# Kernel optimization log

Measured on AMD Instinct MI355X. Metric: run time of the kernel, lower is better.

The kernel has to match this reference:

```python
import math
import jax, jax.numpy as jnp
import numpy as np

N_HEADS = 16
D_EMBED = 1024
D_HEAD = D_EMBED // N_HEADS
B, S = 4, 2048


def setup_inputs() -> dict:
    key = jax.random.key(0)
    k1, k2, k3, k4, k5 = jax.random.split(key, 5)
    scale_in = 1.0 / math.sqrt(D_EMBED)
    return {
        "x": jax.random.normal(k1, (B, S, D_EMBED), dtype=jnp.float32),
        "w_in": jax.random.normal(k2, (3 * D_EMBED, D_EMBED), dtype=jnp.float32) * scale_in,
        "b_in": jax.random.normal(k3, (3 * D_EMBED,), dtype=jnp.float32) * 0.02,
        "w_out": jax.random.normal(k4, (D_EMBED, D_EMBED), dtype=jnp.float32) * scale_in,
        "b_out": jax.random.normal(k5, (D_EMBED,), dtype=jnp.float32) * 0.02,
        "causal_mask": 1,
    }


def reference(x, w_in, b_in, w_out, b_out, causal_mask):
    Bn, Sn, D = x.shape
    # fused QKV projection (torch Linear: x @ W.T + b)
    qkv = x @ w_in.T + b_in                       # (B, S, 3D)
    q, k, v = jnp.split(qkv, 3, axis=-1)
    def to_heads(t):
        return t.reshape(Bn, Sn, N_HEADS, D_HEAD).transpose(0, 2, 1, 3)  # (B,H,S,dh)
    q, k, v = to_heads(q), to_heads(k), to_heads(v)
    # manual scaled dot-product attention, full (B,H,S,S) scores
    scores = jnp.einsum("bhqd,bhkd->bhqk", q, k)
    if causal_mask:
        tri = jnp.triu(jnp.ones((Sn, Sn), dtype=bool), k=1)
        scores = jnp.where(tri, -jnp.inf, scores)
    scores = scores / math.sqrt(D_HEAD)
    weights = jax.nn.softmax(scores, axis=-1)
    out = jnp.einsum("bhqk,bhkd->bhqd", weights, v)  # (B,H,S,dh)
    out = out.transpose(0, 2, 1, 3).reshape(Bn, Sn, D)
    return out @ w_out.T + b_out
```

## Files before the change

### kernel.cpp

```cpp
#include <hip/hip_runtime.h>

typedef __bf16 bf16x8 __attribute__((ext_vector_type(8)));
typedef float  f32x4  __attribute__((ext_vector_type(4)));
typedef unsigned int uint;

__device__ inline unsigned short f2bf(float f) {
  union { float f; unsigned int u; } v; v.f = f;
  unsigned int u = v.u;
  unsigned int r = u + 0x7FFF + ((u >> 16) & 1);
  return (unsigned short)(r >> 16);
}

__device__ inline uint pack_bf16_rhu(float a, float b) {
  uint ua = __builtin_bit_cast(uint, a) + 0x8000u;
  uint ub = __builtin_bit_cast(uint, b) + 0x8000u;
  return __builtin_amdgcn_perm(ub, ua, 0x07060302u);
}

__device__ inline void load_lds16(const unsigned short* g, unsigned short* l) {
  __builtin_amdgcn_global_load_lds(
      (const __attribute__((address_space(1))) uint*)(g),
      (__attribute__((address_space(3))) uint*)(l), 16, 0, 0);
}

__device__ inline void cvt4(const float* in, unsigned short* out) {
  float4 f = *reinterpret_cast<const float4*>(in);
  ushort4 o;
  o.x = f2bf(f.x); o.y = f2bf(f.y); o.z = f2bf(f.z); o.w = f2bf(f.w);
  *reinterpret_cast<ushort4*>(out) = o;
}

__global__ void cvt_all(const float* __restrict__ x, const float* __restrict__ w_in,
                        const float* __restrict__ w_out,
                        unsigned short* __restrict__ x_bf,
                        unsigned short* __restrict__ w_in_bf,
                        unsigned short* __restrict__ w_out_bf) {
  const int n1 = 8192 * 1024, n2 = 3072 * 1024;
  int i = (blockIdx.x * blockDim.x + threadIdx.x) * 4;
  if (i < n1)            cvt4(x + i, x_bf + i);
  else if (i < n1 + n2)  cvt4(w_in + (i - n1), w_in_bf + (i - n1));
  else                   cvt4(w_out + (i - n1 - n2), w_out_bf + (i - n1 - n2));
}

template<bool OUT_BF16, bool VSPLIT>
__global__ __launch_bounds__(256) void gemm_bt128(
    const unsigned short* __restrict__ A,
    const unsigned short* __restrict__ B,
    const float* __restrict__ bias,
    void* __restrict__ Cout,
    unsigned short* __restrict__ vt,
    int M, int N, int K, int ldc, float scale, int ncut)
{
  __shared__ __attribute__((aligned(16))) unsigned short As[128 * 64];
  __shared__ __attribute__((aligned(16))) unsigned short Bs[128 * 64];

  const int t    = threadIdx.x;
  const int wave = t >> 6, lane = t & 63;
  const int l16  = lane & 15, quad = lane >> 4;
  const int wr = wave >> 1, wc = wave & 1;
  const int m0 = blockIdx.y * 128, n0 = blockIdx.x * 128;
  const int l8 = l16 & 7;

  f32x4 acc[4][4] = {};

  for (int k0 = 0; k0 < K; k0 += 64) {
#pragma unroll
    for (int i = 0; i < 4; ++i) {
      int chunk = i * 256 + t;
      int row = chunk >> 3, cb = chunk & 7;
      int gcb = cb ^ (row & 7);
      load_lds16(A + (size_t)(m0 + row) * K + k0 + gcb * 8, As + chunk * 8);
    }
#pragma unroll
    for (int i = 0; i < 4; ++i) {
      int chunk = i * 256 + t;
      int row = chunk >> 3, cb = chunk & 7;
      int gcb = cb ^ (row & 7);
      load_lds16(B + (size_t)(n0 + row) * K + k0 + gcb * 8, Bs + chunk * 8);
    }
    __syncthreads();
#pragma unroll
    for (int ks = 0; ks < 2; ++ks) {
      bf16x8 af[4], bfr[4];
#pragma unroll
      for (int mt = 0; mt < 4; ++mt)
        af[mt] = *(const bf16x8*)(As + (wr * 64 + mt * 16 + l16) * 64 +
                                  (((ks * 4 + quad) ^ l8) << 3));
#pragma unroll
      for (int nt = 0; nt < 4; ++nt)
        bfr[nt] = *(const bf16x8*)(Bs + (wc * 64 + nt * 16 + l16) * 64 +
                                   (((ks * 4 + quad) ^ l8) << 3));
#pragma unroll
      for (int mt = 0; mt < 4; ++mt)
#pragma unroll
        for (int nt = 0; nt < 4; ++nt)
          acc[mt][nt] = __builtin_amdgcn_mfma_f32_16x16x32_bf16(af[mt], bfr[nt], acc[mt][nt], 0, 0, 0);
    }
    __syncthreads();
  }

#pragma unroll
  for (int nt = 0; nt < 4; ++nt) {
    int col = n0 + wc * 64 + nt * 16 + l16;
    float bv = bias[col];
    float mlt = (col < ncut) ? scale : 1.0f;
#pragma unroll
    for (int mt = 0; mt < 4; ++mt) {
      int row0 = m0 + wr * 64 + mt * 16 + quad * 4;
      float v0 = (acc[mt][nt][0] + bv) * mlt;
      float v1 = (acc[mt][nt][1] + bv) * mlt;
      float v2 = (acc[mt][nt][2] + bv) * mlt;
      float v3 = (acc[mt][nt][3] + bv) * mlt;
      if (VSPLIT && col >= 2048) {
        int d = col - 2048, h = d >> 6, dd = d & 63;
        int bb = row0 >> 11, s = row0 & 2047;
        uint2 w;
        w.x = pack_bf16_rhu(v0, v1);
        w.y = pack_bf16_rhu(v2, v3);
        *(uint2*)(vt + ((size_t)((bb * 16 + h) * 64 + dd) * 2048 + s)) = w;
      } else {
#pragma unroll
        for (int r = 0; r < 4; ++r) {
          float v = (r == 0) ? v0 : (r == 1) ? v1 : (r == 2) ? v2 : v3;
          if (OUT_BF16)
            ((unsigned short*)Cout)[(size_t)(row0 + r) * ldc + col] = f2bf(v);
          else
            ((float*)Cout)[(size_t)(row0 + r) * ldc + col] = v;
        }
      }
    }
  }
}

__global__ __launch_bounds__(512) void attn(
    const unsigned short* __restrict__ qkv2,
    const unsigned short* __restrict__ vt,
    unsigned short* __restrict__ y,
    const int* __restrict__ flag)
{
  __shared__ __attribute__((aligned(16))) unsigned short Qs[128 * 64];
  __shared__ __attribute__((aligned(16))) unsigned short Ks[2][64 * 64];
  __shared__ __attribute__((aligned(16))) unsigned short Vs[2][64 * 64];

  const int t    = threadIdx.x;
  const int wave = t >> 6, lane = t & 63;
  const int l16  = lane & 15, quad = lane >> 4;
  const int l8   = l16 & 7;
  const int idx  = blockIdx.x;
  const int bh   = idx & 63;
  const int pair = idx >> 6;
  const int b = bh >> 4, h = bh & 15;
  const int causal = flag[0];

  const unsigned short* Qg  = qkv2 + (size_t)b * 2048 * 2048 + h * 64;
  const unsigned short* Kg  = Qg + 1024;
  const unsigned short* Vtg = vt + (size_t)bh * 64 * 2048;

  const int sr = t >> 2, sg = (t & 3) * 2;
  const int slot0 = sr * 64 + (((sg    ) ^ (sr & 7)) << 3);
  const int slot1 = sr * 64 + (((sg + 1) ^ (sr & 7)) << 3);
  const int kr = t >> 3, kg = t & 7;
  const int kslot = kr * 64 + ((kg ^ (kr & 7)) << 3);

  unsigned short* Ps = Qs;

  for (int half = 0; half < 2; ++half) {
    const int qt = half ? pair : (15 - pair);
    const int q0 = qt * 128;
    const int jmax = causal ? 2 * qt + 1 : 31;

    const unsigned short* kptr = Kg + (size_t)kr * 2048 + kg * 8;
    const unsigned short* vptr = Vtg + (size_t)kr * 2048 + kg * 8;
    uint4 kreg = *(const uint4*)kptr;
    uint4 vreg = *(const uint4*)vptr;
    {
      const unsigned short* src = Qg + (size_t)(q0 + sr) * 2048 + sg * 8;
      *(uint4*)(Qs + slot0) = *(const uint4*)src;
      *(uint4*)(Qs + slot1) = *(const uint4*)(src + 8);
    }
    __syncthreads();
    bf16x8 qf[2];
    qf[0] = *(const bf16x8*)(Qs + (wave * 16 + l16) * 64 + (((0 + quad) ^ l8) << 3));
    qf[1] = *(const bf16x8*)(Qs + (wave * 16 + l16) * 64 + (((4 + quad) ^ l8) << 3));
    __syncthreads();

    *(uint4*)(Ks[0] + kslot) = kreg;
    *(uint4*)(Vs[0] + kslot) = vreg;
    kptr += 64 * 2048;
    vptr += 64;
    if (jmax > 0) {
      kreg = *(const uint4*)kptr;
      vreg = *(const uint4*)vptr;
    }
    __syncthreads();

    f32x4 ot[4] = {};
    float l_lane = 0.f;
    const int q_glob = q0 + wave * 16 + l16;
    const int wq_max = q0 + wave * 16 + 15;

    for (int j = 0; j <= jmax; ++j) {
      const int cur = j & 1;
      if (j < jmax) {
        *(uint4*)(Ks[cur ^ 1] + kslot) = kreg;
        *(uint4*)(Vs[cur ^ 1] + kslot) = vreg;
        if (j + 1 < jmax) {
          kptr += 64 * 2048;
          vptr += 64;
          kreg = *(const uint4*)kptr;
          vreg = *(const uint4*)vptr;
        }
      }

      const bool active = !causal || ((j << 6) <= wq_max);
      if (active) {
        f32x4 st[4] = {};
        __builtin_amdgcn_s_setprio(1);
#pragma unroll
        for (int ks = 0; ks < 2; ++ks) {
#pragma unroll
          for (int mt = 0; mt < 4; ++mt) {
            bf16x8 kf = *(const bf16x8*)(Ks[cur] + (mt * 16 + l16) * 64 +
                                         (((ks * 4 + quad) ^ l8) << 3));
            st[mt] = __builtin_amdgcn_mfma_f32_16x16x32_bf16(kf, qf[ks], st[mt], 0, 0, 0);
          }
        }
        __builtin_amdgcn_s_setprio(0);

        const int kv0 = j << 6;
        const bool diag = (causal != 0) && (kv0 + 63 > q_glob);
#pragma unroll
        for (int mt = 0; mt < 4; ++mt) {
          float p[4];
#pragma unroll
          for (int r = 0; r < 4; ++r) {
            float pv = __builtin_amdgcn_exp2f(st[mt][r]);
            if (diag) {
              int kv = kv0 + mt * 16 + quad * 4 + r;
              if (kv > q_glob) pv = 0.f;
            }
            p[r] = pv;
          }
          l_lane += (p[0] + p[1]) + (p[2] + p[3]);
          uint2 w;
          w.x = pack_bf16_rhu(p[0], p[1]);
          w.y = pack_bf16_rhu(p[2], p[3]);
          *(uint2*)(Ps + (wave * 16 + l16) * 64 +
                    ((((mt * 2 + (quad >> 1)) ^ l8) << 3) + (quad & 1) * 4)) = w;
        }
        __threadfence_block();

        __builtin_amdgcn_s_setprio(1);
#pragma unroll
        for (int ks = 0; ks < 2; ++ks) {
          bf16x8 pf = *(const bf16x8*)(Ps + (wave * 16 + l16) * 64 +
                                       (((ks * 4 + quad) ^ l8) << 3));
#pragma unroll
          for (int mt = 0; mt < 4; ++mt) {
            bf16x8 vf = *(const bf16x8*)(Vs[cur] + (mt * 16 + l16) * 64 +
                                         (((ks * 4 + quad) ^ l8) << 3));
            ot[mt] = __builtin_amdgcn_mfma_f32_16x16x32_bf16(vf, pf, ot[mt], 0, 0, 0);
          }
        }
        __builtin_amdgcn_s_setprio(0);
      }
      __syncthreads();
    }

    l_lane += __shfl_xor(l_lane, 16);
    l_lane += __shfl_xor(l_lane, 32);
    float inv = 1.f / l_lane;

#pragma unroll
    for (int mt = 0; mt < 4; ++mt) {
      uint2 w;
      w.x = pack_bf16_rhu(ot[mt][0] * inv, ot[mt][1] * inv);
      w.y = pack_bf16_rhu(ot[mt][2] * inv, ot[mt][3] * inv);
      *(uint2*)(Ps + (wave * 16 + l16) * 64 +
                ((((mt * 2 + (quad >> 1)) ^ l8) << 3) + (quad & 1) * 4)) = w;
    }
    __syncthreads();
    {
      size_t base = ((size_t)b * 2048 + q0 + sr) * 1024 + h * 64 + sg * 8;
      *(uint4*)(y + base)     = *(const uint4*)(Ps + slot0);
      *(uint4*)(y + base + 8) = *(const uint4*)(Ps + slot1);
    }
    __syncthreads();
  }
}

extern "C" void kernel_launch(void* const* d_in, const int* in_sizes, int n_in,
                              void* d_out, int out_size, void* d_ws, size_t ws_size,
                              hipStream_t stream) {
  const float* x     = (const float*)d_in[0];
  const float* w_in  = (const float*)d_in[1];
  const float* b_in  = (const float*)d_in[2];
  const float* w_out = (const float*)d_in[3];
  const float* b_out = (const float*)d_in[4];
  const int*   cmask = (const int*)d_in[5];

  char* ws = (char*)d_ws;
  unsigned short* x_bf     = (unsigned short*)(ws);
  unsigned short* w_in_bf  = (unsigned short*)(ws + 16777216);
  unsigned short* w_out_bf = (unsigned short*)(ws + 23068672);
  unsigned short* qkv2_bf  = (unsigned short*)(ws + 25165824);
  unsigned short* vt_bf    = (unsigned short*)(ws + 58720256);
  unsigned short* y_bf     = (unsigned short*)(ws + 75497472);

  const int ntot = (8192 + 3072 + 1024) * 1024;
  cvt_all<<<dim3(ntot / 4 / 256), 256, 0, stream>>>(x, w_in, w_out, x_bf, w_in_bf, w_out_bf);

  gemm_bt128<true, true><<<dim3(24, 64), 256, 0, stream>>>(
      x_bf, w_in_bf, b_in, qkv2_bf, vt_bf, 8192, 3072, 1024, 2048,
      0.18033688011112042f, 1024);

  attn<<<dim3(512), 512, 0, stream>>>(qkv2_bf, vt_bf, y_bf, cmask);

  gemm_bt128<false, false><<<dim3(8, 64), 256, 0, stream>>>(
      y_bf, w_out_bf, b_out, d_out, nullptr, 8192, 1024, 1024, 1024, 1.0f, 0);
}
```

Before: 241.8 us.

## Double-buffer LDS in the GEMM with 256x128 tiles and XCD-aware block remap

The bf16 GEMM kernel now uses 512-thread blocks computing 256x128 output tiles. It stages two K-slices into two LDS buffers so global-to-LDS loads overlap MFMA compute, using explicit vmcnt/lgkmcnt waits and raw barriers. Block IDs are also remapped across the 8 XCDs to improve L2 locality. The goal is to hide global load latency and raise reuse of the A tile, at the cost of 96KB of LDS per block, which limits occupancy to one block per CU.

```diff
diff --git a/kernel.cpp b/kernel.cpp
--- a/kernel.cpp
+++ b/kernel.cpp
@@ -43,7 +43,7 @@
 }
 
 template<bool OUT_BF16, bool VSPLIT>
-__global__ __launch_bounds__(256) void gemm_bt128(
+__global__ __launch_bounds__(512, 2) void gemm_bt256(
     const unsigned short* __restrict__ A,
     const unsigned short* __restrict__ B,
     const float* __restrict__ bias,
@@ -51,44 +51,49 @@
     unsigned short* __restrict__ vt,
     int M, int N, int K, int ldc, float scale, int ncut)
 {
-  __shared__ __attribute__((aligned(16))) unsigned short As[128 * 64];
-  __shared__ __attribute__((aligned(16))) unsigned short Bs[128 * 64];
+  __shared__ __attribute__((aligned(16))) unsigned short As[2][256 * 64];
+  __shared__ __attribute__((aligned(16))) unsigned short Bs[2][128 * 64];
 
   const int t    = threadIdx.x;
   const int wave = t >> 6, lane = t & 63;
-  const int l16  = lane & 15, quad = lane >> 4;
-  const int wr = wave >> 1, wc = wave & 1;
-  const int m0 = blockIdx.y * 128, n0 = blockIdx.x * 128;
-  const int l8 = l16 & 7;
+  const int l16  = lane & 15, quad = lane >> 4, l8 = l16 & 7;
+  const int wr   = wave >> 1, wc = wave & 1;
+
+  const int gdx = gridDim.x;
+  int bid = blockIdx.y * gdx + blockIdx.x;
+  const int nwg = gdx * gridDim.y;
+  bid = (bid & 7) * (nwg >> 3) + (bid >> 3);
+  const int m0 = (bid / gdx) * 256;
+  const int n0 = (bid % gdx) * 128;
 
   f32x4 acc[4][4] = {};
 
-  for (int k0 = 0; k0 < K; k0 += 64) {
-#pragma unroll
-    for (int i = 0; i < 4; ++i) {
-      int chunk = i * 256 + t;
-      int row = chunk >> 3, cb = chunk & 7;
-      int gcb = cb ^ (row & 7);
-      load_lds16(A + (size_t)(m0 + row) * K + k0 + gcb * 8, As + chunk * 8);
-    }
-#pragma unroll
-    for (int i = 0; i < 4; ++i) {
-      int chunk = i * 256 + t;
-      int row = chunk >> 3, cb = chunk & 7;
-      int gcb = cb ^ (row & 7);
-      load_lds16(B + (size_t)(n0 + row) * K + k0 + gcb * 8, Bs + chunk * 8);
-    }
-    __syncthreads();
+  auto stage = [&](int kt, unsigned short* Asb, unsigned short* Bsb) {
+#pragma unroll
+    for (int j = 0; j < 4; ++j) {
+      int c = j * 512 + t;
+      int row = c >> 3, gcb = (c & 7) ^ (row & 7);
+      load_lds16(A + (size_t)(m0 + row) * K + kt * 64 + gcb * 8, Asb + c * 8);
+    }
+#pragma unroll
+    for (int j = 0; j < 2; ++j) {
+      int c = j * 512 + t;
+      int row = c >> 3, gcb = (c & 7) ^ (row & 7);
+      load_lds16(B + (size_t)(n0 + row) * K + kt * 64 + gcb * 8, Bsb + c * 8);
+    }
+  };
+
+  auto compute = [&](const unsigned short* Asb, const unsigned short* Bsb) {
 #pragma unroll
     for (int ks = 0; ks < 2; ++ks) {
       bf16x8 af[4], bfr[4];
 #pragma unroll
       for (int mt = 0; mt < 4; ++mt)
-        af[mt] = *(const bf16x8*)(As + (wr * 64 + mt * 16 + l16) * 64 +
+        af[mt] = *(const bf16x8*)(Asb + (wr * 64 + mt * 16 + l16) * 64 +
                                   (((ks * 4 + quad) ^ l8) << 3));
 #pragma unroll
       for (int nt = 0; nt < 4; ++nt)
-        bfr[nt] = *(const bf16x8*)(Bs + (wc * 64 + nt * 16 + l16) * 64 +
+        bfr[nt] = *(const bf16x8*)(Bsb + (wc * 64 + nt * 16 + l16) * 64 +
                                    (((ks * 4 + quad) ^ l8) << 3));
 #pragma unroll
       for (int mt = 0; mt < 4; ++mt)
@@ -96,7 +101,35 @@
         for (int nt = 0; nt < 4; ++nt)
           acc[mt][nt] = __builtin_amdgcn_mfma_f32_16x16x32_bf16(af[mt], bfr[nt], acc[mt][nt], 0, 0, 0);
     }
-    __syncthreads();
+  };
+
+  const int NIT = K >> 7;
+
+  stage(0, As[0], Bs[0]);
+  stage(1, As[1], Bs[1]);
+  asm volatile("s_waitcnt vmcnt(6)" ::: "memory");
+  __builtin_amdgcn_s_barrier();
+
+  for (int i = 0; i < NIT; ++i) {
+    compute(As[0], Bs[0]);
+    asm volatile("s_waitcnt lgkmcnt(0)" ::: "memory");
+    __builtin_amdgcn_s_barrier();
+    if (i < NIT - 1) {
+      stage(2 * i + 2, As[0], Bs[0]);
+      asm volatile("s_waitcnt vmcnt(6)" ::: "memory");
+    } else {
+      asm volatile("s_waitcnt vmcnt(0)" ::: "memory");
+    }
+    __builtin_amdgcn_s_barrier();
+
+    compute(As[1], Bs[1]);
+    if (i < NIT - 1) {
+      asm volatile("s_waitcnt lgkmcnt(0)" ::: "memory");
+      __builtin_amdgcn_s_barrier();
+      stage(2 * i + 3, As[1], Bs[1]);
+      asm volatile("s_waitcnt vmcnt(6)" ::: "memory");
+      __builtin_amdgcn_s_barrier();
+    }
   }
 
 #pragma unroll
@@ -310,12 +343,12 @@
   const int ntot = (8192 + 3072 + 1024) * 1024;
   cvt_all<<<dim3(ntot / 4 / 256), 256, 0, stream>>>(x, w_in, w_out, x_bf, w_in_bf, w_out_bf);
 
-  gemm_bt128<true, true><<<dim3(24, 64), 256, 0, stream>>>(
+  gemm_bt256<true, true><<<dim3(24, 32), 512, 0, stream>>>(
       x_bf, w_in_bf, b_in, qkv2_bf, vt_bf, 8192, 3072, 1024, 2048,
       0.18033688011112042f, 1024);
 
   attn<<<dim3(512), 512, 0, stream>>>(qkv2_bf, vt_bf, y_bf, cmask);
 
-  gemm_bt128<false, false><<<dim3(8, 64), 256, 0, stream>>>(
+  gemm_bt256<false, false><<<dim3(8, 32), 512, 0, stream>>>(
       y_bf, w_out_bf, b_out, d_out, nullptr, 8192, 1024, 1024, 1024, 1.0f, 0);
 }
```

After: 248.0 us. +2.6%, slower.

## Rewrite GEMM as 256x128-tile, 8-wave kernel with triple-buffered LDS pipeline

Applied to the files above, without the earlier changes.

Replaces the 128x128 single-buffered GEMM with a 256x128 tile run by 512 threads. It uses a three-stage LDS ring fed by global_load_lds, so loads for tile k+2 overlap the MFMAs on tile k, and it splits each k-step into two half-steps with barriers and raised wave priority around the MFMA bursts. It also remaps block ids into eight interleaved groups to improve L2 reuse. The cost is much more LDS per block (144 KB), tricky manual vmcnt accounting, and fewer blocks in the grid.

```diff
diff --git a/kernel.cpp b/kernel.cpp
--- a/kernel.cpp
+++ b/kernel.cpp
@@ -43,7 +43,7 @@
 }
 
 template<bool OUT_BF16, bool VSPLIT>
-__global__ __launch_bounds__(256) void gemm_bt128(
+__global__ __launch_bounds__(512, 2) void gemm_bt3(
     const unsigned short* __restrict__ A,
     const unsigned short* __restrict__ B,
     const float* __restrict__ bias,
@@ -51,53 +51,106 @@
     unsigned short* __restrict__ vt,
     int M, int N, int K, int ldc, float scale, int ncut)
 {
-  __shared__ __attribute__((aligned(16))) unsigned short As[128 * 64];
-  __shared__ __attribute__((aligned(16))) unsigned short Bs[128 * 64];
+  __shared__ __attribute__((aligned(16))) unsigned short As3[3][256 * 64];
+  __shared__ __attribute__((aligned(16))) unsigned short Bs3[3][128 * 64];
 
   const int t    = threadIdx.x;
   const int wave = t >> 6, lane = t & 63;
-  const int l16  = lane & 15, quad = lane >> 4;
-  const int wr = wave >> 1, wc = wave & 1;
-  const int m0 = blockIdx.y * 128, n0 = blockIdx.x * 128;
-  const int l8 = l16 & 7;
+  const int l16  = lane & 15, quad = lane >> 4, l8 = l16 & 7;
+  const int wr   = wave >> 1, wc = wave & 1;
+
+  const int gdx = gridDim.x;
+  const int bid0 = blockIdx.y * gdx + blockIdx.x;
+  const int nwg = gdx * gridDim.y;
+  const int bid = (bid0 & 7) * (nwg >> 3) + (bid0 >> 3);
+  const int m0 = (bid / gdx) * 256;
+  const int n0 = (bid % gdx) * 128;
+
+  const int r0  = t >> 3;
+  const int gcb = (t & 7) ^ (r0 & 7);
+  const unsigned short* sA = A + (size_t)(m0 + r0) * K + gcb * 8;
+  const unsigned short* sB = B + (size_t)(n0 + r0) * K + gcb * 8;
+  const int d0 = t * 8;
 
   f32x4 acc[4][4] = {};
-
-  for (int k0 = 0; k0 < K; k0 += 64) {
-#pragma unroll
-    for (int i = 0; i < 4; ++i) {
-      int chunk = i * 256 + t;
-      int row = chunk >> 3, cb = chunk & 7;
-      int gcb = cb ^ (row & 7);
-      load_lds16(A + (size_t)(m0 + row) * K + k0 + gcb * 8, As + chunk * 8);
-    }
-#pragma unroll
-    for (int i = 0; i < 4; ++i) {
-      int chunk = i * 256 + t;
-      int row = chunk >> 3, cb = chunk & 7;
-      int gcb = cb ^ (row & 7);
-      load_lds16(B + (size_t)(n0 + row) * K + k0 + gcb * 8, Bs + chunk * 8);
-    }
-    __syncthreads();
-#pragma unroll
-    for (int ks = 0; ks < 2; ++ks) {
-      bf16x8 af[4], bfr[4];
-#pragma unroll
-      for (int mt = 0; mt < 4; ++mt)
-        af[mt] = *(const bf16x8*)(As + (wr * 64 + mt * 16 + l16) * 64 +
-                                  (((ks * 4 + quad) ^ l8) << 3));
-#pragma unroll
-      for (int nt = 0; nt < 4; ++nt)
-        bfr[nt] = *(const bf16x8*)(Bs + (wc * 64 + nt * 16 + l16) * 64 +
-                                   (((ks * 4 + quad) ^ l8) << 3));
-#pragma unroll
-      for (int mt = 0; mt < 4; ++mt)
-#pragma unroll
-        for (int nt = 0; nt < 4; ++nt)
-          acc[mt][nt] = __builtin_amdgcn_mfma_f32_16x16x32_bf16(af[mt], bfr[nt], acc[mt][nt], 0, 0, 0);
-    }
-    __syncthreads();
+  bf16x8 af[4][2], bfr[4][2];
+
+#define STAGE_A(KT, H, DST)                                                   \
+  { load_lds16(sA + (size_t)((H) * 128     ) * K + (KT) * 64,                 \
+               (DST) + (H) * 8192 + d0);                                      \
+    load_lds16(sA + (size_t)((H) * 128 + 64) * K + (KT) * 64,                 \
+               (DST) + (H) * 8192 + 4096 + d0); }
+#define STAGE_B(KT, H, DST)                                                   \
+    load_lds16(sB + (size_t)((H) * 64) * K + (KT) * 64, (DST) + (H) * 4096 + d0);
+#define LOAD_AF(SRC)                                                          \
+  { _Pragma("unroll")                                                         \
+    for (int m = 0; m < 4; ++m) {                                             \
+      _Pragma("unroll")                                                       \
+      for (int ks = 0; ks < 2; ++ks)                                          \
+        af[m][ks] = *(const bf16x8*)((SRC) + (wr * 64 + m * 16 + l16) * 64 +  \
+                                     (((ks * 4 + quad) ^ l8) << 3)); } }
+#define LOAD_BF2(SRC, N0)                                                     \
+  { _Pragma("unroll")                                                         \
+    for (int dn = 0; dn < 2; ++dn) {                                          \
+      _Pragma("unroll")                                                       \
+      for (int ks = 0; ks < 2; ++ks)                                          \
+        bfr[(N0) + dn][ks] = *(const bf16x8*)((SRC) +                         \
+            (wc * 64 + ((N0) + dn) * 16 + l16) * 64 +                         \
+            (((ks * 4 + quad) ^ l8) << 3)); } }
+#define MMA2(N0)                                                              \
+  { __builtin_amdgcn_s_setprio(1);                                            \
+    _Pragma("unroll")                                                         \
+    for (int ks = 0; ks < 2; ++ks) {                                          \
+      _Pragma("unroll")                                                       \
+      for (int m = 0; m < 4; ++m) {                                           \
+        _Pragma("unroll")                                                     \
+        for (int dn = 0; dn < 2; ++dn)                                        \
+          acc[m][(N0) + dn] = __builtin_amdgcn_mfma_f32_16x16x32_bf16(        \
+              af[m][ks], bfr[(N0) + dn][ks], acc[m][(N0) + dn], 0, 0, 0);     \
+      } }                                                                     \
+    __builtin_amdgcn_s_setprio(0); }
+
+  const int NT = K >> 6;
+
+  STAGE_A(0, 0, As3[0]); STAGE_B(0, 0, Bs3[0]);
+  STAGE_A(0, 1, As3[0]); STAGE_B(0, 1, Bs3[0]);
+  STAGE_A(1, 0, As3[1]); STAGE_B(1, 0, Bs3[1]);
+  STAGE_A(1, 1, As3[1]); STAGE_B(1, 1, Bs3[1]);
+  asm volatile("s_waitcnt vmcnt(6)" ::: "memory");
+  __builtin_amdgcn_s_barrier();
+
+  int p = 0;
+  for (int tt = 0; tt < NT; ++tt) {
+    const unsigned short* Ap = As3[p];
+    const unsigned short* Bp = Bs3[p];
+    const int q = (p + 2 < 3) ? p + 2 : p - 1;
+    unsigned short* Aq = As3[q];
+    unsigned short* Bq = Bs3[q];
+    const bool st = (tt + 2 < NT);
+
+    LOAD_AF(Ap);
+    LOAD_BF2(Bp, 0);
+    if (st) { STAGE_A(tt + 2, 0, Aq); STAGE_B(tt + 2, 0, Bq); }
+    __builtin_amdgcn_s_barrier();
+    MMA2(0);
+    __builtin_amdgcn_s_barrier();
+
+    LOAD_BF2(Bp, 2);
+    if (st) { STAGE_A(tt + 2, 1, Aq); STAGE_B(tt + 2, 1, Bq); }
+    __builtin_amdgcn_s_barrier();
+    MMA2(2);
+    if (tt < NT - 2) { asm volatile("s_waitcnt vmcnt(6)" ::: "memory"); }
+    else             { asm volatile("s_waitcnt vmcnt(0)" ::: "memory"); }
+    __builtin_amdgcn_s_barrier();
+
+    p = (p + 1 < 3) ? p + 1 : 0;
   }
+
+#undef STAGE_A
+#undef STAGE_B
+#undef LOAD_AF
+#undef LOAD_BF2
+#undef MMA2
 
 #pragma unroll
   for (int nt = 0; nt < 4; ++nt) {
@@ -310,12 +363,12 @@
   const int ntot = (8192 + 3072 + 1024) * 1024;
   cvt_all<<<dim3(ntot / 4 / 256), 256, 0, stream>>>(x, w_in, w_out, x_bf, w_in_bf, w_out_bf);
 
-  gemm_bt128<true, true><<<dim3(24, 64), 256, 0, stream>>>(
+  gemm_bt3<true, true><<<dim3(24, 32), 512, 0, stream>>>(
       x_bf, w_in_bf, b_in, qkv2_bf, vt_bf, 8192, 3072, 1024, 2048,
       0.18033688011112042f, 1024);
 
   attn<<<dim3(512), 512, 0, stream>>>(qkv2_bf, vt_bf, y_bf, cmask);
 
-  gemm_bt128<false, false><<<dim3(8, 64), 256, 0, stream>>>(
+  gemm_bt3<false, false><<<dim3(8, 32), 512, 0, stream>>>(
       y_bf, w_out_bf, b_out, d_out, nullptr, 8192, 1024, 1024, 1024, 1.0f, 0);
 }
```

Result: slower. 265.8 us (+9.9%).

## Halve attention block to 4 waves, each handling 32 query rows

Applied to the files above, without the earlier changes.

The attention kernel now launches 256 threads instead of 512. Each wave processes two 16-row query groups, so every K and V fragment read from LDS feeds two MFMAs instead of one. This cuts LDS read traffic per unit of compute, but doubles per-wave registers for accumulators and scores and halves the waves available to hide latency. Each thread also loads twice as many K/V/Q elements.

```diff
diff --git a/kernel.cpp b/kernel.cpp
--- a/kernel.cpp
+++ b/kernel.cpp
@@ -132,7 +132,7 @@
   }
 }
 
-__global__ __launch_bounds__(512) void attn(
+__global__ __launch_bounds__(256) void attn(
     const unsigned short* __restrict__ qkv2,
     const unsigned short* __restrict__ vt,
     unsigned short* __restrict__ y,
@@ -171,50 +171,67 @@
 
     const unsigned short* kptr = Kg + (size_t)kr * 2048 + kg * 8;
     const unsigned short* vptr = Vtg + (size_t)kr * 2048 + kg * 8;
-    uint4 kreg = *(const uint4*)kptr;
-    uint4 vreg = *(const uint4*)vptr;
+    uint4 kreg0 = *(const uint4*)kptr;
+    uint4 kreg1 = *(const uint4*)(kptr + 32 * 2048);
+    uint4 vreg0 = *(const uint4*)vptr;
+    uint4 vreg1 = *(const uint4*)(vptr + 32 * 2048);
     {
-      const unsigned short* src = Qg + (size_t)(q0 + sr) * 2048 + sg * 8;
-      *(uint4*)(Qs + slot0) = *(const uint4*)src;
-      *(uint4*)(Qs + slot1) = *(const uint4*)(src + 8);
-    }
-    __syncthreads();
-    bf16x8 qf[2];
-    qf[0] = *(const bf16x8*)(Qs + (wave * 16 + l16) * 64 + (((0 + quad) ^ l8) << 3));
-    qf[1] = *(const bf16x8*)(Qs + (wave * 16 + l16) * 64 + (((4 + quad) ^ l8) << 3));
-    __syncthreads();
-
-    *(uint4*)(Ks[0] + kslot) = kreg;
-    *(uint4*)(Vs[0] + kslot) = vreg;
+      const unsigned short* src  = Qg + (size_t)(q0 + sr) * 2048 + sg * 8;
+      const unsigned short* src2 = src + 64 * 2048;
+      *(uint4*)(Qs + slot0)        = *(const uint4*)src;
+      *(uint4*)(Qs + slot1)        = *(const uint4*)(src + 8);
+      *(uint4*)(Qs + slot0 + 4096) = *(const uint4*)src2;
+      *(uint4*)(Qs + slot1 + 4096) = *(const uint4*)(src2 + 8);
+    }
+    __syncthreads();
+    bf16x8 qf[2][2];
+#pragma unroll
+    for (int g = 0; g < 2; ++g)
+#pragma unroll
+      for (int ks = 0; ks < 2; ++ks)
+        qf[g][ks] = *(const bf16x8*)(Qs + (wave * 32 + g * 16 + l16) * 64 +
+                                     (((ks * 4 + quad) ^ l8) << 3));
+    __syncthreads();
+
+    *(uint4*)(Ks[0] + kslot)        = kreg0;
+    *(uint4*)(Ks[0] + kslot + 2048) = kreg1;
+    *(uint4*)(Vs[0] + kslot)        = vreg0;
+    *(uint4*)(Vs[0] + kslot + 2048) = vreg1;
     kptr += 64 * 2048;
     vptr += 64;
     if (jmax > 0) {
-      kreg = *(const uint4*)kptr;
-      vreg = *(const uint4*)vptr;
-    }
-    __syncthreads();
-
-    f32x4 ot[4] = {};
-    float l_lane = 0.f;
-    const int q_glob = q0 + wave * 16 + l16;
-    const int wq_max = q0 + wave * 16 + 15;
+      kreg0 = *(const uint4*)kptr;
+      kreg1 = *(const uint4*)(kptr + 32 * 2048);
+      vreg0 = *(const uint4*)vptr;
+      vreg1 = *(const uint4*)(vptr + 32 * 2048);
+    }
+    __syncthreads();
+
+    f32x4 ot[2][4] = {};
+    float l_lane[2] = {0.f, 0.f};
+    const int q_glob = q0 + wave * 32 + l16;
+    const int wq_max = q0 + wave * 32 + 31;
 
     for (int j = 0; j <= jmax; ++j) {
       const int cur = j & 1;
       if (j < jmax) {
-        *(uint4*)(Ks[cur ^ 1] + kslot) = kreg;
-        *(uint4*)(Vs[cur ^ 1] + kslot) = vreg;
+        *(uint4*)(Ks[cur ^ 1] + kslot)        = kreg0;
+        *(uint4*)(Ks[cur ^ 1] + kslot + 2048) = kreg1;
+        *(uint4*)(Vs[cur ^ 1] + kslot)        = vreg0;
+        *(uint4*)(Vs[cur ^ 1] + kslot + 2048) = vreg1;
         if (j + 1 < jmax) {
           kptr += 64 * 2048;
           vptr += 64;
-          kreg = *(const uint4*)kptr;
-          vreg = *(const uint4*)vptr;
+          kreg0 = *(const uint4*)kptr;
+          kreg1 = *(const uint4*)(kptr + 32 * 2048);
+          vreg0 = *(const uint4*)vptr;
+          vreg1 = *(const uint4*)(vptr + 32 * 2048);
         }
       }
 
       const bool active = !causal || ((j << 6) <= wq_max);
       if (active) {
-        f32x4 st[4] = {};
+        f32x4 st[2][4] = {};
         __builtin_amdgcn_s_setprio(1);
 #pragma unroll
         for (int ks = 0; ks < 2; ++ks) {
@@ -222,44 +239,51 @@
           for (int mt = 0; mt < 4; ++mt) {
             bf16x8 kf = *(const bf16x8*)(Ks[cur] + (mt * 16 + l16) * 64 +
                                          (((ks * 4 + quad) ^ l8) << 3));
-            st[mt] = __builtin_amdgcn_mfma_f32_16x16x32_bf16(kf, qf[ks], st[mt], 0, 0, 0);
+            st[0][mt] = __builtin_amdgcn_mfma_f32_16x16x32_bf16(kf, qf[0][ks], st[0][mt], 0, 0, 0);
+            st[1][mt] = __builtin_amdgcn_mfma_f32_16x16x32_bf16(kf, qf[1][ks], st[1][mt], 0, 0, 0);
           }
         }
         __builtin_amdgcn_s_setprio(0);
 
         const int kv0 = j << 6;
-        const bool diag = (causal != 0) && (kv0 + 63 > q_glob);
-#pragma unroll
-        for (int mt = 0; mt < 4; ++mt) {
-          float p[4];
-#pragma unroll
-          for (int r = 0; r < 4; ++r) {
-            float pv = __builtin_amdgcn_exp2f(st[mt][r]);
-            if (diag) {
-              int kv = kv0 + mt * 16 + quad * 4 + r;
-              if (kv > q_glob) pv = 0.f;
+#pragma unroll
+        for (int g = 0; g < 2; ++g) {
+          const int qg = q_glob + g * 16;
+          const bool diag = (causal != 0) && (kv0 + 63 > qg);
+          const int prow = (wave * 32 + g * 16 + l16) * 64;
+#pragma unroll
+          for (int mt = 0; mt < 4; ++mt) {
+            float p[4];
+#pragma unroll
+            for (int r = 0; r < 4; ++r) {
+              float pv = __builtin_amdgcn_exp2f(st[g][mt][r]);
+              if (diag) {
+                int kv = kv0 + mt * 16 + quad * 4 + r;
+                if (kv > qg) pv = 0.f;
+              }
+              p[r] = pv;
             }
-            p[r] = pv;
+            l_lane[g] += (p[0] + p[1]) + (p[2] + p[3]);
+            uint2 w;
+            w.x = pack_bf16_rhu(p[0], p[1]);
+            w.y = pack_bf16_rhu(p[2], p[3]);
+            *(uint2*)(Ps + prow +
+                      ((((mt * 2 + (quad >> 1)) ^ l8) << 3) + (quad & 1) * 4)) = w;
           }
-          l_lane += (p[0] + p[1]) + (p[2] + p[3]);
-          uint2 w;
-          w.x = pack_bf16_rhu(p[0], p[1]);
-          w.y = pack_bf16_rhu(p[2], p[3]);
-          *(uint2*)(Ps + (wave * 16 + l16) * 64 +
-                    ((((mt * 2 + (quad >> 1)) ^ l8) << 3) + (quad & 1) * 4)) = w;
         }
         __threadfence_block();
 
         __builtin_amdgcn_s_setprio(1);
 #pragma unroll
         for (int ks = 0; ks < 2; ++ks) {
-          bf16x8 pf = *(const bf16x8*)(Ps + (wave * 16 + l16) * 64 +
-                                       (((ks * 4 + quad) ^ l8) << 3));
+          const int gofs = ((ks * 4 + quad) ^ l8) << 3;
+          bf16x8 pf0 = *(const bf16x8*)(Ps + (wave * 32 + l16) * 64 + gofs);
+          bf16x8 pf1 = *(const bf16x8*)(Ps + (wave * 32 + 16 + l16) * 64 + gofs);
 #pragma unroll
           for (int mt = 0; mt < 4; ++mt) {
-            bf16x8 vf = *(const bf16x8*)(Vs[cur] + (mt * 16 + l16) * 64 +
-                                         (((ks * 4 + quad) ^ l8) << 3));
-            ot[mt] = __builtin_amdgcn_mfma_f32_16x16x32_bf16(vf, pf, ot[mt], 0, 0, 0);
+            bf16x8 vf = *(const bf16x8*)(Vs[cur] + (mt * 16 + l16) * 64 + gofs);
+            ot[0][mt] = __builtin_amdgcn_mfma_f32_16x16x32_bf16(vf, pf0, ot[0][mt], 0, 0, 0);
+            ot[1][mt] = __builtin_amdgcn_mfma_f32_16x16x32_bf16(vf, pf1, ot[1][mt], 0, 0, 0);
           }
         }
         __builtin_amdgcn_s_setprio(0);
@@ -267,23 +291,30 @@
       __syncthreads();
     }
 
-    l_lane += __shfl_xor(l_lane, 16);
-    l_lane += __shfl_xor(l_lane, 32);
-    float inv = 1.f / l_lane;
-
-#pragma unroll
-    for (int mt = 0; mt < 4; ++mt) {
-      uint2 w;
-      w.x = pack_bf16_rhu(ot[mt][0] * inv, ot[mt][1] * inv);
-      w.y = pack_bf16_rhu(ot[mt][2] * inv, ot[mt][3] * inv);
-      *(uint2*)(Ps + (wave * 16 + l16) * 64 +
-                ((((mt * 2 + (quad >> 1)) ^ l8) << 3) + (quad & 1) * 4)) = w;
+#pragma unroll
+    for (int g = 0; g < 2; ++g) {
+      float l = l_lane[g];
+      l += __shfl_xor(l, 16);
+      l += __shfl_xor(l, 32);
+      float inv = 1.f / l;
+      const int prow = (wave * 32 + g * 16 + l16) * 64;
+#pragma unroll
+      for (int mt = 0; mt < 4; ++mt) {
+        uint2 w;
+        w.x = pack_bf16_rhu(ot[g][mt][0] * inv, ot[g][mt][1] * inv);
+        w.y = pack_bf16_rhu(ot[g][mt][2] * inv, ot[g][mt][3] * inv);
+        *(uint2*)(Ps + prow +
+                  ((((mt * 2 + (quad >> 1)) ^ l8) << 3) + (quad & 1) * 4)) = w;
+      }
     }
     __syncthreads();
     {
-      size_t base = ((size_t)b * 2048 + q0 + sr) * 1024 + h * 64 + sg * 8;
-      *(uint4*)(y + base)     = *(const uint4*)(Ps + slot0);
-      *(uint4*)(y + base + 8) = *(const uint4*)(Ps + slot1);
+      size_t base0 = ((size_t)b * 2048 + q0 + sr) * 1024 + h * 64 + sg * 8;
+      size_t base1 = base0 + (size_t)64 * 1024;
+      *(uint4*)(y + base0)     = *(const uint4*)(Ps + slot0);
+      *(uint4*)(y + base0 + 8) = *(const uint4*)(Ps + slot1);
+      *(uint4*)(y + base1)     = *(const uint4*)(Ps + slot0 + 4096);
+      *(uint4*)(y + base1 + 8) = *(const uint4*)(Ps + slot1 + 4096);
     }
     __syncthreads();
   }
@@ -314,7 +345,7 @@
       x_bf, w_in_bf, b_in, qkv2_bf, vt_bf, 8192, 3072, 1024, 2048,
       0.18033688011112042f, 1024);
 
-  attn<<<dim3(512), 512, 0, stream>>>(qkv2_bf, vt_bf, y_bf, cmask);
+  attn<<<dim3(512), 256, 0, stream>>>(qkv2_bf, vt_bf, y_bf, cmask);
 
   gemm_bt128<false, false><<<dim3(8, 64), 256, 0, stream>>>(
       y_bf, w_out_bf, b_out, d_out, nullptr, 8192, 1024, 1024, 1024, 1.0f, 0);
```

Result: slower. 262.0 us (+8.4%).
